# Performance work log

Measured on AMD Instinct MI355X. Metric: run time of the kernel, lower is better.

The kernel has to match this reference:

```python
import jax, jax.numpy as jnp
import numpy as np

B, NP, DIM = 32, 1369, 768
NCLS, K = 200, 5
C = NCLS + 1          # n_classes + background
H = W = 37            # sqrt(NP)
GAMMA = 0.99
SCALE = 4.0
SINKHORN_ITERS = 3
PCA_ITERS = 10
PCA_THRESH = 0.5
EPS = 1e-8


def _l2norm(x):
    return x / jnp.clip(jnp.linalg.norm(x, axis=-1, keepdims=True), EPS)


def setup_inputs() -> dict:
    key = jax.random.key(0)
    k1, k2, k3 = jax.random.split(key, 3)
    patch_tokens = jax.random.normal(k1, (B, NP, DIM), dtype=jnp.float32)
    labels = jax.random.randint(k2, (B,), 0, NCLS)
    prototypes = 0.02 * jax.random.normal(k3, (C, K, DIM), dtype=jnp.float32)  # trunc_normal std=0.02 approx
    sa = jnp.full((NCLS, K), 0.5, dtype=jnp.float32)
    scale = jnp.asarray(SCALE, dtype=jnp.float32)
    return {"patch_tokens": patch_tokens, "labels": labels,
            "prototypes": prototypes, "sa": sa, "scale": scale}


def reference(patch_tokens, labels, prototypes, sa, scale):
    # --- cosine patch-prototype similarity ---
    tok_n = _l2norm(patch_tokens)                 # [B, NP, D]
    pro_n = _l2norm(prototypes)                   # [C, K, D]
    logits = scale * jnp.einsum('bnd,ckd->bnck', tok_n, pro_n)  # [B, NP, C, K]

    # --- avg pooling + 'sa' classification head ---
    image_logits = logits.mean(axis=1)            # [B, C, K]
    sa_w = jax.nn.softmax(sa, axis=-1) * K        # [NCLS, K]
    class_logits = (image_logits[:, :NCLS, :] * sa_w).sum(axis=-1)  # [B, NCLS]

    # --- PCA pseudo patch labels (power iteration, q=1, centered) ---
    X = jax.lax.stop_gradient(patch_tokens).reshape(-1, DIM)  # [N, D]
    Xc = X - X.mean(axis=0, keepdims=True)
    v = jax.random.normal(jax.random.key(42), (DIM,), dtype=jnp.float32)
    for _ in range(PCA_ITERS):
        u = Xc @ v
        v = Xc.T @ u
        v = v / jnp.clip(jnp.linalg.norm(v), EPS)
    u = Xc @ v
    U = u / jnp.clip(jnp.linalg.norm(u), EPS)     # leading left singular vector
    U_scaled = (U - U.min()) / jnp.clip(U.max() - U.min(), EPS)
    U_img = U_scaled.reshape(B, H, W)
    pseudo = jnp.where(U_img <= PCA_THRESH,
                       labels[:, None, None],
                       C - 1).astype(jnp.int32)   # [B, H, W]

    # --- online clustering: masked sinkhorn vectorized over classes ---
    flat_lab = pseudo.reshape(-1)                 # [N]
    cls_ids = jnp.arange(C)
    mask = (flat_lab[:, None] == cls_ids[None, :]).astype(jnp.float32)  # [N, C]
    Nc = mask.sum(axis=0)                         # [C] fg patch count per class
    Lf = jax.lax.stop_gradient(logits).reshape(-1, C, K)
    Q = jnp.exp(Lf) * mask[:, :, None]            # [N, C, K], zero outside class mask
    Q = Q / jnp.clip(Q.sum(axis=(0, 2)), EPS)[None, :, None]
    Ncc = jnp.clip(Nc, 1.0)
    for _ in range(SINKHORN_ITERS):
        Q = Q / jnp.clip(Q.sum(axis=0), EPS)[None] / K           # col normalize
        Q = Q / jnp.clip(Q.sum(axis=2, keepdims=True), EPS) / Ncc[None, :, None]  # row normalize
    Q = Q * Nc[None, :, None]
    tok_flat = jax.lax.stop_gradient(tok_n).reshape(-1, DIM)
    P_new = jnp.einsum('nck,nd->ckd', Q, tok_flat)               # [C, K, D]
    updated = GAMMA * prototypes + (1.0 - GAMMA) * P_new          # momentum update
    present = jnp.isin(cls_ids, labels)                           # classes in this batch
    new_prototypes = jnp.where(present[:, None, None], updated, prototypes)

    return (logits, image_logits, class_logits, pseudo, new_prototypes)
```

## Files before the change

### kernel.cpp

```cpp
#include <hip/hip_runtime.h>

constexpr int   BB    = 32;
constexpr int   NPP   = 1369;
constexpr int   DIMC  = 768;
constexpr int   NCLSC = 200;
constexpr int   KP    = 5;
constexpr int   CC    = 201;
constexpr int   CKC   = 1005;
constexpr int   NPAD  = 1024;
constexpr int   NTOK  = BB * NPP;
constexpr float EPSF  = 1e-8f;
constexpr int   PWIN  = 128;
constexpr int   MTILES = 343;
constexpr int   NSLAB = 4;

typedef __attribute__((ext_vector_type(8))) short bf16x8;
typedef __attribute__((ext_vector_type(4))) float f32x4;

constexpr size_t O_LOG = 0;
constexpr size_t O_IMG = (size_t)NTOK * CKC;
constexpr size_t O_CLS = O_IMG + (size_t)BB * CKC;
constexpr size_t O_PSE = O_CLS + (size_t)BB * NCLSC;
constexpr size_t O_PRO = O_PSE + (size_t)NTOK;

constexpr size_t W_PRONBF = 0;
constexpr size_t W_INVN   = W_PRONBF + (size_t)NPAD*DIMC/2;
constexpr size_t W_MU     = W_INVN + NTOK;
constexpr size_t W_COLS   = W_MU + 2*DIMC;
constexpr size_t W_VBUF   = W_COLS + 2*NSLAB*DIMC;
constexpr size_t W_SSUM   = W_VBUF + 2*11*NSLAB*DIMC;
constexpr size_t W_TSUM   = W_SSUM + 128;
constexpr size_t W_NC     = W_TSUM + CC;
constexpr size_t W_FILL   = W_NC + CC;
constexpr size_t W_PRES   = W_FILL + CC;
constexpr size_t ZG_LEN   = (W_PRES + CC) - W_COLS;
constexpr size_t W_CSQ    = W_PRES + CC;
constexpr size_t W_U      = ((W_CSQ + CKC) + 1) & ~(size_t)1;
constexpr size_t W_PART   = W_U + 2*NTOK;
constexpr size_t W_SCAL   = W_PART + 2*1536;
constexpr size_t W_Q      = W_SCAL + 16;
constexpr size_t W_PNEW   = W_Q + (size_t)NTOK*KP;
constexpr size_t W_PLAB   = W_PNEW + (size_t)CC*KP*DIMC;
constexpr size_t W_OFFS   = W_PLAB + NTOK;
constexpr size_t W_RLST   = W_OFFS + 256;
constexpr size_t W_XBF    = ((W_RLST + NTOK) + 3) & ~(size_t)3;
constexpr size_t W_END_BIG  = W_XBF + (size_t)(NTOK + 128)*DIMC/2;
constexpr size_t W_PRON32   = W_XBF;
constexpr size_t W_END_FALL = W_PRON32 + (size_t)CKC*DIMC;

__device__ __forceinline__ unsigned short f2bf(float x) {
    unsigned u = __float_as_uint(x);
    unsigned r = (u + 0x7fffu + ((u >> 16) & 1u)) >> 16;
    return (unsigned short)r;
}

typedef __attribute__((address_space(3))) unsigned int as3_u32;
typedef __attribute__((address_space(1))) unsigned int as1_u32;
__device__ __forceinline__ void gload16(const unsigned short* g, unsigned short* l) {
    __builtin_amdgcn_global_load_lds((as1_u32*)g, (as3_u32*)l, 16, 0, 0);
}

__global__ void fill_zero(float* p, int n) {
    int i = blockIdx.x * 256 + threadIdx.x;
    if (i < n) p[i] = 0.0f;
}

__global__ __launch_bounds__(256) void tok_stats(const float* __restrict__ X,
                                                 float* __restrict__ invn,
                                                 double* __restrict__ colsD,
                                                 unsigned short* __restrict__ xbf) {
    __shared__ double csh[4][768];
    const int tid  = threadIdx.x;
    const int lane = tid & 63;
    const int wid  = tid >> 6;
    const int gw   = blockIdx.x * 4 + wid;
    double cacc[3][4];
    #pragma unroll
    for (int j = 0; j < 3; j++)
        #pragma unroll
        for (int t = 0; t < 4; t++) cacc[j][t] = 0.0;
    for (int n = gw; n < NTOK; n += 4096) {
        const float4* row = (const float4*)(X + (size_t)n * DIMC);
        float s = 0.0f;
        float4 xv[3];
        #pragma unroll
        for (int j = 0; j < 3; j++) {
            xv[j] = row[lane + 64*j];
            s = fmaf(xv[j].x, xv[j].x, s); s = fmaf(xv[j].y, xv[j].y, s);
            s = fmaf(xv[j].z, xv[j].z, s); s = fmaf(xv[j].w, xv[j].w, s);
            cacc[j][0] += (double)xv[j].x; cacc[j][1] += (double)xv[j].y;
            cacc[j][2] += (double)xv[j].z; cacc[j][3] += (double)xv[j].w;
        }
        if (xbf) {
            unsigned short* orow = xbf + (size_t)n * DIMC;
            #pragma unroll
            for (int j = 0; j < 3; j++) {
                ushort4 pk;
                pk.x = f2bf(xv[j].x); pk.y = f2bf(xv[j].y);
                pk.z = f2bf(xv[j].z); pk.w = f2bf(xv[j].w);
                *(ushort4*)(orow + 4*(lane + 64*j)) = pk;
            }
        }
        #pragma unroll
        for (int o = 32; o >= 1; o >>= 1) s += __shfl_xor(s, o);
        if (lane == 0) invn[n] = 1.0f / fmaxf(sqrtf(s), EPSF);
    }
    #pragma unroll
    for (int j = 0; j < 3; j++)
        #pragma unroll
        for (int t = 0; t < 4; t++)
            csh[wid][4*lane + 256*j + t] = cacc[j][t];
    __syncthreads();
    const int slab = blockIdx.x & (NSLAB - 1);
    for (int c = tid; c < 768; c += 256)
        atomicAdd(&colsD[slab * 768 + c], csh[0][c] + csh[1][c] + csh[2][c] + csh[3][c]);
}

__global__ __launch_bounds__(256) void proto_norm(const float* __restrict__ P,
                                                  unsigned short* __restrict__ pbf,
                                                  float* __restrict__ p32) {
    const int lane = threadIdx.x & 63;
    const int gw   = blockIdx.x * 4 + (threadIdx.x >> 6);
    for (int j = gw; j < NPAD; j += 256) {
        unsigned short* obf = pbf + (size_t)j * DIMC;
        if (j >= CKC) {
            #pragma unroll
            for (int t = 0; t < 12; t++) obf[lane + 64*t] = 0;
            continue;
        }
        const float* row = P + (size_t)j * DIMC;
        float x[12]; float s = 0.0f;
        #pragma unroll
        for (int t = 0; t < 12; t++) { x[t] = row[lane + 64*t]; s = fmaf(x[t], x[t], s); }
        #pragma unroll
        for (int o = 32; o >= 1; o >>= 1) s += __shfl_xor(s, o);
        float nrm = fmaxf(sqrtf(s), EPSF);
        #pragma unroll
        for (int t = 0; t < 12; t++) {
            float nv = x[t] / nrm;
            obf[lane + 64*t] = f2bf(nv);
            if (p32) p32[(size_t)j * DIMC + lane + 64*t] = nv;
        }
    }
}

__global__ __launch_bounds__(256) void logits_gemm(
        const unsigned short* __restrict__ Xbf,
        const unsigned short* __restrict__ Pbf,
        const float* __restrict__ invn,
        const float* __restrict__ scale_p,
        float* __restrict__ out,
        float* __restrict__ img) {
    __shared__ unsigned short As[128 * 32];
    __shared__ unsigned short Bs[128 * 32];
    const int b   = blockIdx.x;
    const int swz = (b & 7) * MTILES + (b >> 3);
    const int row_t = swz >> 3, col_t = swz & 7;
    const int row0 = row_t * 128, col0 = col_t * 128;
    const int tid = threadIdx.x, lane = tid & 63, wid = tid >> 6;
    const int wm = (wid >> 1) * 64, wn = (wid & 1) * 64;
    const int fr = lane & 15, fq = lane >> 4;

    f32x4 acc[4][4] = {};

    const int w32 = wid * 32;
    const int lrow = lane >> 2;
    const int gch = ((lane & 3) ^ ((lrow ^ (lrow >> 2)) & 3)) * 8;
    const unsigned short* aS0 = Xbf + (size_t)(row0 + w32 + lrow) * DIMC + gch;
    const unsigned short* aS1 = aS0 + (size_t)16 * DIMC;
    const unsigned short* bS0 = Pbf + (size_t)(col0 + w32 + lrow) * DIMC + gch;
    const unsigned short* bS1 = bS0 + (size_t)16 * DIMC;
    unsigned short* aD0 = &As[(w32)      * 32];
    unsigned short* aD1 = &As[(w32 + 16) * 32];
    unsigned short* bD0 = &Bs[(w32)      * 32];
    unsigned short* bD1 = &Bs[(w32 + 16) * 32];

    const int rc = (fq ^ ((fr ^ (fr >> 2)) & 3)) * 8;

    for (int ks = 0; ks < DIMC / 32; ks++) {
        __syncthreads();
        gload16(aS0 + ks * 32, aD0);
        gload16(aS1 + ks * 32, aD1);
        gload16(bS0 + ks * 32, bD0);
        gload16(bS1 + ks * 32, bD1);
        __syncthreads();
        bf16x8 af[4], bfr[4];
        #pragma unroll
        for (int m = 0; m < 4; m++)
            af[m] = *(const bf16x8*)(As + (wm + m * 16 + fr) * 32 + rc);
        #pragma unroll
        for (int n = 0; n < 4; n++)
            bfr[n] = *(const bf16x8*)(Bs + (wn + n * 16 + fr) * 32 + rc);
        #pragma unroll
        for (int m = 0; m < 4; m++)
            #pragma unroll
            for (int n = 0; n < 4; n++)
                acc[m][n] = __builtin_amdgcn_mfma_f32_16x16x32_bf16(af[m], bfr[n], acc[m][n], 0, 0, 0);
    }

    const float sc = *scale_p;
    #pragma unroll
    for (int m = 0; m < 4; m++) {
        const int rbase = row0 + wm + m * 16 + fq * 4;
        float fin[4];
        #pragma unroll
        for (int rr = 0; rr < 4; rr++) {
            int rrow = rbase + rr;
            fin[rr] = (rrow < NTOK) ? sc * invn[rrow] : 0.0f;
        }
        const int strip0 = row0 + wm + m * 16;
        const bool sameImg = ((strip0 / NPP) == ((strip0 + 15) / NPP)) && (strip0 + 15) < NTOK;
        const int bimg = strip0 / NPP;
        #pragma unroll
        for (int n = 0; n < 4; n++) {
            const int col = col0 + wn + n * 16 + fr;
            const bool cok = col < CKC;
            float csum = 0.0f;
            #pragma unroll
            for (int rr = 0; rr < 4; rr++) {
                int rrow = rbase + rr;
                float v = fin[rr] * acc[m][n][rr];
                if (cok && rrow < NTOK) out[(size_t)rrow * CKC + col] = v;
                csum += v;
            }
            if (sameImg) {
                csum += __shfl_xor(csum, 16);
                csum += __shfl_xor(csum, 32);
                if (lane < 16 && cok) atomicAdd(&img[bimg * CKC + col], csum);
            } else if (cok) {
                #pragma unroll
                for (int rr = 0; rr < 4; rr++) {
                    int rrow = rbase + rr;
                    if (rrow < NTOK)
                        atomicAdd(&img[(rrow / NPP) * CKC + col], fin[rr] * acc[m][n][rr]);
                }
            }
        }
    }
}

__global__ __launch_bounds__(256) void gemm_logits(const float* __restrict__ X,
                                                   const float* __restrict__ Bn,
                                                   const float* __restrict__ invn,
                                                   const float* __restrict__ scale_p,
                                                   float* __restrict__ out) {
    __shared__ float As[32][68];
    __shared__ float Bs[32][68];
    const int tid = threadIdx.x;
    const int tx = tid & 15, ty = tid >> 4;
    const int row0 = blockIdx.x * 64;
    const int col0 = blockIdx.y * 64;
    const int lm = tid >> 2;
    const int kb = (tid & 3) * 8;
    float acc[4][4] = {};
    for (int k0 = 0; k0 < DIMC; k0 += 32) {
        float a[8], b[8];
        int ar = row0 + lm;
        if (ar < NTOK) {
            const float* ap = X + (size_t)ar * DIMC + k0 + kb;
            #pragma unroll
            for (int j = 0; j < 8; j++) a[j] = ap[j];
        } else {
            #pragma unroll
            for (int j = 0; j < 8; j++) a[j] = 0.0f;
        }
        int bc = col0 + lm;
        if (bc < CKC) {
            const float* bp = Bn + (size_t)bc * DIMC + k0 + kb;
            #pragma unroll
            for (int j = 0; j < 8; j++) b[j] = bp[j];
        } else {
            #pragma unroll
            for (int j = 0; j < 8; j++) b[j] = 0.0f;
        }
        __syncthreads();
        #pragma unroll
        for (int j = 0; j < 8; j++) As[kb + j][lm] = a[j];
        #pragma unroll
        for (int j = 0; j < 8; j++) Bs[kb + j][lm] = b[j];
        __syncthreads();
        #pragma unroll
        for (int kk = 0; kk < 32; kk++) {
            float av[4], bv[4];
            #pragma unroll
            for (int i = 0; i < 4; i++) av[i] = As[kk][ty*4 + i];
            #pragma unroll
            for (int j = 0; j < 4; j++) bv[j] = Bs[kk][tx*4 + j];
            #pragma unroll
            for (int i = 0; i < 4; i++)
                #pragma unroll
                for (int j = 0; j < 4; j++)
                    acc[i][j] = fmaf(av[i], bv[j], acc[i][j]);
        }
    }
    const float sc = *scale_p;
    #pragma unroll
    for (int i = 0; i < 4; i++) {
        int r = row0 + ty*4 + i;
        if (r >= NTOK) continue;
        float f = sc * invn[r];
        float* orow = out + (size_t)r * CKC;
        #pragma unroll
        for (int j = 0; j < 4; j++) {
            int c = col0 + tx*4 + j;
            if (c < CKC) orow[c] = f * acc[i][j];
        }
    }
}

__global__ void img_reduce(const float* __restrict__ logits, float* __restrict__ img) {
    int b = blockIdx.x, jc = blockIdx.y, nc = blockIdx.z;
    int j = jc * 256 + threadIdx.x;
    if (j >= CKC) return;
    int p0 = nc * 172, p1 = min(NPP, p0 + 172);
    const float* base = logits + (size_t)b * NPP * CKC + j;
    float s = 0.0f;
    for (int p = p0; p < p1; p++) s += base[(size_t)p * CKC];
    atomicAdd(&img[b * CKC + j], s);
}

__global__ __launch_bounds__(256) void img_final(float* __restrict__ img,
                                                 const float* __restrict__ sa,
                                                 float* __restrict__ cls) {
    int b = blockIdx.x;
    for (int i = threadIdx.x; i < CKC; i += 256)
        img[b * CKC + i] = img[b * CKC + i] / 1369.0f;
    __syncthreads();
    for (int c = threadIdx.x; c < NCLSC; c += 256) {
        float vv[KP]; float mx = -3.4e38f;
        #pragma unroll
        for (int k = 0; k < KP; k++) { vv[k] = sa[c * KP + k]; mx = fmaxf(mx, vv[k]); }
        float e[KP]; float s = 0.0f;
        #pragma unroll
        for (int k = 0; k < KP; k++) { e[k] = expf(vv[k] - mx); s += e[k]; }
        float cl = 0.0f;
        #pragma unroll
        for (int k = 0; k < KP; k++) {
            float sw = e[k] / s * 5.0f;
            cl += img[b * CKC + c * KP + k] * sw;
        }
        cls[b * NCLSC + c] = cl;
    }
}

__global__ void mu_final(const double* __restrict__ colsD, double* __restrict__ mu) {
    int d = threadIdx.x;
    mu[d] = (colsD[d] + colsD[768 + d] + colsD[1536 + d] + colsD[2304 + d]) / (double)NTOK;
}

__device__ __forceinline__ float bits_to_normal(unsigned bits) {
    float f = __uint_as_float((bits >> 9) | 0x3f800000u) - 1.0f;
    const float lo = -0.99999994f;
    float u = f * 2.0f + lo;
    u = fmaxf(lo, u);
    float w = -log1pf(-u * u);
    float p;
    if (w < 5.0f) {
        w -= 2.5f;
        p = 2.81022636e-08f;
        p = fmaf(p, w, 3.43273939e-07f);
        p = fmaf(p, w, -3.5233877e-06f);
        p = fmaf(p, w, -4.39150654e-06f);
        p = fmaf(p, w, 0.00021858087f);
        p = fmaf(p, w, -0.00125372503f);
        p = fmaf(p, w, -0.00417768164f);
        p = fmaf(p, w, 0.246640727f);
        p = fmaf(p, w, 1.50140941f);
    } else {
        w = sqrtf(w) - 3.0f;
        p = -0.000200214257f;
        p = fmaf(p, w, 0.000100950558f);
        p = fmaf(p, w, 0.00134934322f);
        p = fmaf(p, w, -0.00367342844f);
        p = fmaf(p, w, 0.00573950773f);
        p = fmaf(p, w, -0.0076224613f);
        p = fmaf(p, w, 0.00943887047f);
        p = fmaf(p, w, 1.00167406f);
        p = fmaf(p, w, 2.83297682f);
    }
    return 1.41421356237f * (p * u);
}

#define TF_ROUND(r) { x0 += x1; x1 = (x1 << r) | (x1 >> (32 - r)); x1 ^= x0; }
__global__ void v0_gen(double* __restrict__ v) {
    int i = blockIdx.x * 256 + threadIdx.x;
    if (i >= DIMC) return;
    unsigned x0 = 0u, x1 = (unsigned)i;
    const unsigned k0 = 0u, k1 = 42u, k2 = k0 ^ k1 ^ 0x1BD11BDAu;
    x0 += k0; x1 += k1;
    TF_ROUND(13) TF_ROUND(15) TF_ROUND(26) TF_ROUND(6)
    x0 += k1; x1 += k2 + 1u;
    TF_ROUND(17) TF_ROUND(29) TF_ROUND(16) TF_ROUND(24)
    x0 += k2; x1 += k0 + 2u;
    TF_ROUND(13) TF_ROUND(15) TF_ROUND(26) TF_ROUND(6)
    x0 += k0; x1 += k1 + 3u;
    TF_ROUND(17) TF_ROUND(29) TF_ROUND(16) TF_ROUND(24)
    x0 += k1; x1 += k2 + 4u;
    TF_ROUND(13) TF_ROUND(15) TF_ROUND(26) TF_ROUND(6)
    x0 += k2; x1 += k0 + 5u;
    v[i] = (double)bits_to_normal(x0 ^ x1);
}

__global__ __launch_bounds__(256) void pca_pass(const float* __restrict__ X,
                                                const double* __restrict__ mu,
                                                const double* __restrict__ vraw,
                                                const double* __restrict__ Sin,
                                                double* __restrict__ vnext,
                                                double* __restrict__ Snext) {
    __shared__ double wacc[4][768];
    __shared__ double redw[4];
    const int tid = threadIdx.x, lane = tid & 63, wid = tid >> 6;
    const double S = Sin[0] + Sin[1] + Sin[2] + Sin[3];
    double ver[3][4];
    double mv = 0.0;
    #pragma unroll
    for (int j = 0; j < 3; j++)
        #pragma unroll
        for (int t = 0; t < 4; t++) {
            int c = 4*lane + 256*j + t;
            double x = (vraw[c] + vraw[768 + c] + vraw[1536 + c] + vraw[2304 + c]) - S * mu[c];
            ver[j][t] = x;
            mv += mu[c] * x;
        }
    #pragma unroll
    for (int o = 32; o >= 1; o >>= 1) mv += __shfl_xor(mv, o);
    const double muv = mv;

    double acc[3][4] = {};
    double usum = 0.0;
    const int gw = blockIdx.x * 4 + wid;
    for (int n0 = gw; n0 < NTOK; n0 += 4096) {
        const int n1 = n0 + 2048;
        const bool h1 = (n1 < NTOK);
        const float4* r0 = (const float4*)(X + (size_t)n0 * DIMC);
        const float4* r1 = (const float4*)(X + (size_t)(h1 ? n1 : n0) * DIMC);
        float4 xa[3], xb[3];
        #pragma unroll
        for (int j = 0; j < 3; j++) xa[j] = r0[lane + 64*j];
        #pragma unroll
        for (int j = 0; j < 3; j++) xb[j] = r1[lane + 64*j];
        double s0 = 0.0, s1 = 0.0;
        #pragma unroll
        for (int j = 0; j < 3; j++) {
            s0 = fma((double)xa[j].x, ver[j][0], s0);
            s0 = fma((double)xa[j].y, ver[j][1], s0);
            s0 = fma((double)xa[j].z, ver[j][2], s0);
            s0 = fma((double)xa[j].w, ver[j][3], s0);
            s1 = fma((double)xb[j].x, ver[j][0], s1);
            s1 = fma((double)xb[j].y, ver[j][1], s1);
            s1 = fma((double)xb[j].z, ver[j][2], s1);
            s1 = fma((double)xb[j].w, ver[j][3], s1);
        }
        #pragma unroll
        for (int o = 32; o >= 1; o >>= 1) { s0 += __shfl_xor(s0, o); s1 += __shfl_xor(s1, o); }
        double uu0 = s0 - muv;
        usum += uu0;
        #pragma unroll
        for (int j = 0; j < 3; j++) {
            acc[j][0] = fma((double)xa[j].x, uu0, acc[j][0]);
            acc[j][1] = fma((double)xa[j].y, uu0, acc[j][1]);
            acc[j][2] = fma((double)xa[j].z, uu0, acc[j][2]);
            acc[j][3] = fma((double)xa[j].w, uu0, acc[j][3]);
        }
        if (h1) {
            double uu1 = s1 - muv;
            usum += uu1;
            #pragma unroll
            for (int j = 0; j < 3; j++) {
                acc[j][0] = fma((double)xb[j].x, uu1, acc[j][0]);
                acc[j][1] = fma((double)xb[j].y, uu1, acc[j][1]);
                acc[j][2] = fma((double)xb[j].z, uu1, acc[j][2]);
                acc[j][3] = fma((double)xb[j].w, uu1, acc[j][3]);
            }
        }
    }
    #pragma unroll
    for (int j = 0; j < 3; j++)
        #pragma unroll
        for (int t = 0; t < 4; t++)
            wacc[wid][4*lane + 256*j + t] = acc[j][t];
    if (lane == 0) redw[wid] = usum;
    __syncthreads();
    const int slab = blockIdx.x & (NSLAB - 1);
    for (int c = tid; c < 768; c += 256)
        atomicAdd(&vnext[slab * 768 + c], wacc[0][c] + wacc[1][c] + wacc[2][c] + wacc[3][c]);
    if (tid == 0) atomicAdd(&Snext[slab], redw[0] + redw[1] + redw[2] + redw[3]);
}

__global__ __launch_bounds__(256) void u_final(const float* __restrict__ X,
                                               const double* __restrict__ mu,
                                               const double* __restrict__ vraw,
                                               const double* __restrict__ Sin,
                                               double* __restrict__ u,
                                               double* __restrict__ part) {
    __shared__ double wmin[4], wmax[4], wss[4];
    const int tid = threadIdx.x, lane = tid & 63, wid = tid >> 6;
    const double S = Sin[0] + Sin[1] + Sin[2] + Sin[3];
    double ver[3][4];
    double mv = 0.0;
    #pragma unroll
    for (int j = 0; j < 3; j++)
        #pragma unroll
        for (int t = 0; t < 4; t++) {
            int c = 4*lane + 256*j + t;
            double x = (vraw[c] + vraw[768 + c] + vraw[1536 + c] + vraw[2304 + c]) - S * mu[c];
            ver[j][t] = x;
            mv += mu[c] * x;
        }
    #pragma unroll
    for (int o = 32; o >= 1; o >>= 1) mv += __shfl_xor(mv, o);
    const double muv = mv;
    double lmin = 1e300, lmax = -1e300, lss = 0.0;
    for (int n = blockIdx.x * 4 + wid; n < NTOK; n += 2048) {
        const float4* row = (const float4*)(X + (size_t)n * DIMC);
        double s = 0.0;
        #pragma unroll
        for (int j = 0; j < 3; j++) {
            float4 xv = row[lane + 64*j];
            s = fma((double)xv.x, ver[j][0], s);
            s = fma((double)xv.y, ver[j][1], s);
            s = fma((double)xv.z, ver[j][2], s);
            s = fma((double)xv.w, ver[j][3], s);
        }
        #pragma unroll
        for (int o = 32; o >= 1; o >>= 1) s += __shfl_xor(s, o);
        double uu = s - muv;
        if (lane == 0) {
            u[n] = uu;
            lmin = fmin(lmin, uu); lmax = fmax(lmax, uu); lss = fma(uu, uu, lss);
        }
    }
    if (lane == 0) { wmin[wid] = lmin; wmax[wid] = lmax; wss[wid] = lss; }
    __syncthreads();
    if (tid == 0) {
        part[blockIdx.x]        = fmin(fmin(wmin[0], wmin[1]), fmin(wmin[2], wmin[3]));
        part[512 + blockIdx.x]  = fmax(fmax(wmax[0], wmax[1]), fmax(wmax[2], wmax[3]));
        part[1024 + blockIdx.x] = wss[0] + wss[1] + wss[2] + wss[3];
    }
}

__global__ __launch_bounds__(512) void final_scalars(const double* __restrict__ part,
                                                     double* __restrict__ scal,
                                                     const int* __restrict__ labels,
                                                     int* __restrict__ pres) {
    __shared__ double rmin[512], rmax[512], rss[512];
    int t = threadIdx.x;
    rmin[t] = part[t]; rmax[t] = part[512 + t]; rss[t] = part[1024 + t];
    __syncthreads();
    for (int s = 256; s > 0; s >>= 1) {
        if (t < s) {
            rmin[t] = fmin(rmin[t], rmin[t + s]);
            rmax[t] = fmax(rmax[t], rmax[t + s]);
            rss[t] += rss[t + s];
        }
        __syncthreads();
    }
    if (t == 0) {
        double nrm = fmax(sqrt(rss[0]), 1e-8);
        double Umin = rmin[0] / nrm;
        double Umax = rmax[0] / nrm;
        scal[1] = nrm;
        scal[2] = Umin;
        scal[3] = fmax(Umax - Umin, 1e-8);
    }
    if (t < BB) pres[labels[t]] = 1;
}

__global__ __launch_bounds__(256) void pseudo_kernel(
        const double* __restrict__ u, const double* __restrict__ scal,
        const int* __restrict__ labels, float* __restrict__ pse,
        int* __restrict__ plab, int* __restrict__ Nc) {
    __shared__ int hist[CC];
    const int tid = threadIdx.x;
    for (int c = tid; c < CC; c += 256) hist[c] = 0;
    __syncthreads();
    int n = blockIdx.x * 256 + tid;
    if (n < NTOK) {
        double U  = u[n] / scal[1];
        double Us = (U - scal[2]) / scal[3];
        int lab = (Us <= 0.5) ? labels[n / NPP] : (CC - 1);
        pse[n] = (float)lab;
        plab[n] = lab;
        atomicAdd(&hist[lab], 1);
    }
    __syncthreads();
    for (int c = tid; c < CC; c += 256)
        if (hist[c] > 0) atomicAdd(&Nc[c], hist[c]);
}

__global__ void offs_scan(const int* __restrict__ Nc, int* __restrict__ offs) {
    if (threadIdx.x == 0) {
        int s = 0;
        for (int c = 0; c < CC; c++) { offs[c] = s; s += Nc[c]; }
        offs[CC] = s;
    }
}

__global__ __launch_bounds__(256) void scatter_rows(
        const int* __restrict__ plab, const int* __restrict__ offs,
        int* __restrict__ fill, int* __restrict__ rlist) {
    __shared__ int hist[CC];
    __shared__ int base[CC];
    const int tid = threadIdx.x;
    for (int c = tid; c < CC; c += 256) hist[c] = 0;
    __syncthreads();
    int n = blockIdx.x * 256 + tid;
    int lab = -1, posl = 0;
    if (n < NTOK) {
        lab = plab[n];
        posl = atomicAdd(&hist[lab], 1);
    }
    __syncthreads();
    for (int c = tid; c < CC; c += 256) {
        int h = hist[c];
        if (h > 0) base[c] = atomicAdd(&fill[c], h);
    }
    __syncthreads();
    if (n < NTOK) rlist[offs[lab] + base[lab] + posl] = n;
}

__global__ __launch_bounds__(256) void sinkhorn_fused(
        const float* __restrict__ logits,
        const int* __restrict__ offs,
        const int* __restrict__ rlist,
        float* __restrict__ qseg) {
    const int c  = blockIdx.x;
    const int i0 = offs[c], i1 = offs[c + 1];
    const int cnt = i1 - i0;
    if (cnt <= 0) return;
    const int tid = threadIdx.x;
    __shared__ float cs[KP];
    __shared__ float redk[KP][4];

    for (int i = i0 + tid; i < i1; i += 256) {
        int n = rlist[i];
        const float* lp = logits + (size_t)n * CKC + c * KP;
        #pragma unroll
        for (int k = 0; k < KP; k++) qseg[(size_t)i * KP + k] = expf(lp[k]);
    }
    const float Ncc = fmaxf((float)cnt, 1.0f);
    for (int it = 0; it < 3; it++) {
        __syncthreads();
        float lc[KP] = {};
        for (int i = i0 + tid; i < i1; i += 256) {
            #pragma unroll
            for (int k = 0; k < KP; k++) lc[k] += qseg[(size_t)i * KP + k];
        }
        #pragma unroll
        for (int k = 0; k < KP; k++) {
            float v = lc[k];
            #pragma unroll
            for (int o = 32; o >= 1; o >>= 1) v += __shfl_xor(v, o);
            if ((tid & 63) == 0) redk[k][tid >> 6] = v;
        }
        __syncthreads();
        if (tid == 0) {
            #pragma unroll
            for (int k = 0; k < KP; k++)
                cs[k] = fmaxf(redk[k][0] + redk[k][1] + redk[k][2] + redk[k][3], EPSF) * 5.0f;
        }
        __syncthreads();
        float inv_cs[KP];
        #pragma unroll
        for (int k = 0; k < KP; k++) inv_cs[k] = 1.0f / cs[k];
        const float outsc = (it == 2) ? ((float)cnt / Ncc) : (1.0f / Ncc);
        for (int i = i0 + tid; i < i1; i += 256) {
            float v[KP]; float rs = 0.0f;
            #pragma unroll
            for (int k = 0; k < KP; k++) { v[k] = qseg[(size_t)i*KP + k] * inv_cs[k]; rs += v[k]; }
            float f = outsc / fmaxf(rs, EPSF);
            #pragma unroll
            for (int k = 0; k < KP; k++) qseg[(size_t)i*KP + k] = v[k] * f;
        }
    }
}

__global__ __launch_bounds__(256) void pnew_partial(
        const float* __restrict__ X,
        const float* __restrict__ invn,
        const float* __restrict__ qseg,
        const int* __restrict__ offs,
        const int* __restrict__ rlist,
        const int* __restrict__ plab,
        float* __restrict__ Pnew) {
    const int d = blockIdx.y * 256 + threadIdx.x;
    const int fgEnd = offs[CC - 1];
    int i0 = blockIdx.x * PWIN;
    if (i0 >= fgEnd) return;
    int i1 = min(i0 + PWIN, fgEnd);
    int curlab = -1;
    float acc[KP] = {};
    for (int i = i0; i < i1; i++) {
        int n = rlist[i];
        int lab = plab[n];
        if (lab != curlab) {
            if (curlab >= 0) {
                #pragma unroll
                for (int k = 0; k < KP; k++)
                    atomicAdd(&Pnew[((size_t)curlab * KP + k) * DIMC + d], acc[k]);
            }
            curlab = lab;
            #pragma unroll
            for (int k = 0; k < KP; k++) acc[k] = 0.0f;
        }
        float x = X[(size_t)n * DIMC + d] * invn[n];
        #pragma unroll
        for (int k = 0; k < KP; k++) acc[k] = fmaf(qseg[(size_t)i * KP + k], x, acc[k]);
    }
    if (curlab >= 0) {
        #pragma unroll
        for (int k = 0; k < KP; k++)
            atomicAdd(&Pnew[((size_t)curlab * KP + k) * DIMC + d], acc[k]);
    }
}

__global__ void proto_out(const float* __restrict__ proto, const float* __restrict__ Pnew,
                          const int* __restrict__ pres, float* __restrict__ outp) {
    int idx = blockIdx.x * 256 + threadIdx.x;
    if (idx >= CC * KP * DIMC) return;
    int c = idx / (KP * DIMC);
    float p = proto[idx];
    float r = p;
    if (pres[c]) {
        const float g = 0.99f;
        r = g * p + (1.0f - g) * Pnew[idx];
    }
    outp[idx] = r;
}

extern "C" void kernel_launch(void* const* d_in, const int* in_sizes, int n_in,
                              void* d_out, int out_size, void* d_ws, size_t ws_size,
                              hipStream_t stream) {
    const float* X      = (const float*)d_in[0];
    const int*   labels = (const int*)  d_in[1];
    const float* proto  = (const float*)d_in[2];
    const float* sa     = (const float*)d_in[3];
    const float* scale  = (const float*)d_in[4];
    float* out = (float*)d_out;
    float* ws  = (float*)d_ws;
    const bool big = ws_size >= W_END_BIG * sizeof(float);
    if (!big && ws_size < W_END_FALL * sizeof(float)) return;

    unsigned short* pronbf = (unsigned short*)(ws + W_PRONBF);
    float*  invn  = ws + W_INVN;
    double* mu    = (double*)(ws + W_MU);
    double* colsD = (double*)(ws + W_COLS);
    double* vbuf  = (double*)(ws + W_VBUF);
    double* Ssum  = (double*)(ws + W_SSUM);
    int*    Nc    = (int*)(ws + W_NC);
    int*    fill  = (int*)(ws + W_FILL);
    int*    pres  = (int*)(ws + W_PRES);
    double* u     = (double*)(ws + W_U);
    double* part  = (double*)(ws + W_PART);
    double* scal  = (double*)(ws + W_SCAL);
    float*  qseg  = ws + W_Q;
    float*  Pnew  = ws + W_PNEW;
    int*    plab  = (int*)(ws + W_PLAB);
    int*    offs  = (int*)(ws + W_OFFS);
    int*    rlist = (int*)(ws + W_RLST);
    unsigned short* xbf = big ? (unsigned short*)(ws + W_XBF) : nullptr;
    float*  pron32 = big ? nullptr : (ws + W_PRON32);

    fill_zero<<<((int)ZG_LEN + 255) / 256, 256, 0, stream>>>(ws + W_COLS, (int)ZG_LEN);
    fill_zero<<<(CC * KP * DIMC + 255) / 256, 256, 0, stream>>>(Pnew, CC * KP * DIMC);
    fill_zero<<<(BB * CKC + 255) / 256, 256, 0, stream>>>(out + O_IMG, BB * CKC);

    tok_stats<<<1024, 256, 0, stream>>>(X, invn, colsD, xbf);
    proto_norm<<<64, 256, 0, stream>>>(proto, pronbf, pron32);
    if (big) {
        logits_gemm<<<MTILES * 8, 256, 0, stream>>>(xbf, pronbf, invn, scale,
                                                    out + O_LOG, out + O_IMG);
    } else {
        gemm_logits<<<dim3(685, 16), 256, 0, stream>>>(X, pron32, invn, scale, out + O_LOG);
        img_reduce<<<dim3(32, 4, 8), 256, 0, stream>>>(out + O_LOG, out + O_IMG);
    }
    img_final<<<32, 256, 0, stream>>>(out + O_IMG, sa, out + O_CLS);

    mu_final<<<1, 768, 0, stream>>>(colsD, mu);
    v0_gen<<<3, 256, 0, stream>>>(vbuf);
    for (int t = 0; t < 10; t++) {
        pca_pass<<<512, 256, 0, stream>>>(X, mu,
            vbuf + (size_t)t * NSLAB * DIMC, Ssum + t * NSLAB,
            vbuf + (size_t)(t + 1) * NSLAB * DIMC, Ssum + (t + 1) * NSLAB);
    }
    u_final<<<512, 256, 0, stream>>>(X, mu,
        vbuf + (size_t)10 * NSLAB * DIMC, Ssum + 10 * NSLAB, u, part);
    final_scalars<<<1, 512, 0, stream>>>(part, scal, labels, pres);
    pseudo_kernel<<<172, 256, 0, stream>>>(u, scal, labels, out + O_PSE, plab, Nc);

    offs_scan<<<1, 64, 0, stream>>>(Nc, offs);
    scatter_rows<<<172, 256, 0, stream>>>(plab, offs, fill, rlist);
    sinkhorn_fused<<<NCLSC, 256, 0, stream>>>(out + O_LOG, offs, rlist, qseg);
    pnew_partial<<<dim3((NTOK + PWIN - 1) / PWIN, 3), 256, 0, stream>>>(
        X, invn, qseg, offs, rlist, plab, Pnew);
    proto_out<<<(CC * KP * DIMC + 255) / 256, 256, 0, stream>>>(proto, Pnew, pres, out + O_PRO);
}
```

Measured before the change: 599.0 us.

## Double GEMM K-tile to 64 and widen PCA passes to 8 slabs

The logits GEMM now stages 64-wide K slices in LDS with an XOR swizzle over 8 chunks. Each tile feeds two MFMA sub-steps, which halves the number of barrier pairs per K loop. The PCA power-iteration passes launch twice as many blocks and spread their atomics over 8 partial slabs instead of 4, to raise occupancy and cut atomic contention. LDS use per GEMM block doubles, and the reductions now sum 8 partials. One risk is that tok_stats' column partials may still be written for 4 slabs while mu_final now reads 8.

```diff
diff --git a/kernel.cpp b/kernel.cpp
--- a/kernel.cpp
+++ b/kernel.cpp
@@ -12,7 +12,7 @@
 constexpr float EPSF  = 1e-8f;
 constexpr int   PWIN  = 128;
 constexpr int   MTILES = 343;
-constexpr int   NSLAB = 4;
+constexpr int   NSLAB = 8;
 
 typedef __attribute__((ext_vector_type(8))) short bf16x8;
 typedef __attribute__((ext_vector_type(4))) float f32x4;
@@ -29,7 +29,7 @@
 constexpr size_t W_COLS   = W_MU + 2*DIMC;
 constexpr size_t W_VBUF   = W_COLS + 2*NSLAB*DIMC;
 constexpr size_t W_SSUM   = W_VBUF + 2*11*NSLAB*DIMC;
-constexpr size_t W_TSUM   = W_SSUM + 128;
+constexpr size_t W_TSUM   = W_SSUM + 256;
 constexpr size_t W_NC     = W_TSUM + CC;
 constexpr size_t W_FILL   = W_NC + CC;
 constexpr size_t W_PRES   = W_FILL + CC;
@@ -151,8 +151,8 @@
         const float* __restrict__ scale_p,
         float* __restrict__ out,
         float* __restrict__ img) {
-    __shared__ unsigned short As[128 * 32];
-    __shared__ unsigned short Bs[128 * 32];
+    __shared__ unsigned short As[128 * 64];
+    __shared__ unsigned short Bs[128 * 64];
     const int b   = blockIdx.x;
     const int swz = (b & 7) * MTILES + (b >> 3);
     const int row_t = swz >> 3, col_t = swz & 7;
@@ -164,38 +164,36 @@
     f32x4 acc[4][4] = {};
 
     const int w32 = wid * 32;
-    const int lrow = lane >> 2;
-    const int gch = ((lane & 3) ^ ((lrow ^ (lrow >> 2)) & 3)) * 8;
-    const unsigned short* aS0 = Xbf + (size_t)(row0 + w32 + lrow) * DIMC + gch;
-    const unsigned short* aS1 = aS0 + (size_t)16 * DIMC;
-    const unsigned short* bS0 = Pbf + (size_t)(col0 + w32 + lrow) * DIMC + gch;
-    const unsigned short* bS1 = bS0 + (size_t)16 * DIMC;
-    unsigned short* aD0 = &As[(w32)      * 32];
-    unsigned short* aD1 = &As[(w32 + 16) * 32];
-    unsigned short* bD0 = &Bs[(w32)      * 32];
-    unsigned short* bD1 = &Bs[(w32 + 16) * 32];
-
-    const int rc = (fq ^ ((fr ^ (fr >> 2)) & 3)) * 8;
-
-    for (int ks = 0; ks < DIMC / 32; ks++) {
+    const int lr8 = lane >> 3;
+    const int lch = (lane & 7) ^ lr8;
+    const unsigned short* aBase = Xbf + (size_t)(row0 + w32 + lr8) * DIMC + lch * 8;
+    const unsigned short* bBase = Pbf + (size_t)(col0 + w32 + lr8) * DIMC + lch * 8;
+
+    for (int ks = 0; ks < DIMC / 64; ks++) {
         __syncthreads();
-        gload16(aS0 + ks * 32, aD0);
-        gload16(aS1 + ks * 32, aD1);
-        gload16(bS0 + ks * 32, bD0);
-        gload16(bS1 + ks * 32, bD1);
+        #pragma unroll
+        for (int i = 0; i < 4; i++) {
+            gload16(aBase + (size_t)(8 * i) * DIMC + ks * 64, &As[(w32 + 8 * i) * 64]);
+            gload16(bBase + (size_t)(8 * i) * DIMC + ks * 64, &Bs[(w32 + 8 * i) * 64]);
+        }
         __syncthreads();
-        bf16x8 af[4], bfr[4];
-        #pragma unroll
-        for (int m = 0; m < 4; m++)
-            af[m] = *(const bf16x8*)(As + (wm + m * 16 + fr) * 32 + rc);
-        #pragma unroll
-        for (int n = 0; n < 4; n++)
-            bfr[n] = *(const bf16x8*)(Bs + (wn + n * 16 + fr) * 32 + rc);
-        #pragma unroll
-        for (int m = 0; m < 4; m++)
+        #pragma unroll
+        for (int kk = 0; kk < 2; kk++) {
+            bf16x8 af[4], bfr[4];
+            #pragma unroll
+            for (int m = 0; m < 4; m++)
+                af[m] = *(const bf16x8*)(As + (wm + m * 16 + fr) * 64 +
+                                         (((kk << 2) | fq) ^ (fr & 7)) * 8);
             #pragma unroll
             for (int n = 0; n < 4; n++)
-                acc[m][n] = __builtin_amdgcn_mfma_f32_16x16x32_bf16(af[m], bfr[n], acc[m][n], 0, 0, 0);
+                bfr[n] = *(const bf16x8*)(Bs + (wn + n * 16 + fr) * 64 +
+                                          (((kk << 2) | fq) ^ (fr & 7)) * 8);
+            #pragma unroll
+            for (int m = 0; m < 4; m++)
+                #pragma unroll
+                for (int n = 0; n < 4; n++)
+                    acc[m][n] = __builtin_amdgcn_mfma_f32_16x16x32_bf16(af[m], bfr[n], acc[m][n], 0, 0, 0);
+        }
     }
 
     const float sc = *scale_p;
@@ -345,7 +343,10 @@
 
 __global__ void mu_final(const double* __restrict__ colsD, double* __restrict__ mu) {
     int d = threadIdx.x;
-    mu[d] = (colsD[d] + colsD[768 + d] + colsD[1536 + d] + colsD[2304 + d]) / (double)NTOK;
+    double s = 0.0;
+    #pragma unroll
+    for (int k = 0; k < NSLAB; k++) s += colsD[k * 768 + d];
+    mu[d] = s / (double)NTOK;
 }
 
 __device__ __forceinline__ float bits_to_normal(unsigned bits) {
@@ -410,7 +411,9 @@
     __shared__ double wacc[4][768];
     __shared__ double redw[4];
     const int tid = threadIdx.x, lane = tid & 63, wid = tid >> 6;
-    const double S = Sin[0] + Sin[1] + Sin[2] + Sin[3];
+    double S = 0.0;
+    #pragma unroll
+    for (int k = 0; k < NSLAB; k++) S += Sin[k];
     double ver[3][4];
     double mv = 0.0;
     #pragma unroll
@@ -418,7 +421,10 @@
         #pragma unroll
         for (int t = 0; t < 4; t++) {
             int c = 4*lane + 256*j + t;
-            double x = (vraw[c] + vraw[768 + c] + vraw[1536 + c] + vraw[2304 + c]) - S * mu[c];
+            double vr = 0.0;
+            #pragma unroll
+            for (int k = 0; k < NSLAB; k++) vr += vraw[k * 768 + c];
+            double x = vr - S * mu[c];
             ver[j][t] = x;
             mv += mu[c] * x;
         }
@@ -429,8 +435,8 @@
     double acc[3][4] = {};
     double usum = 0.0;
     const int gw = blockIdx.x * 4 + wid;
-    for (int n0 = gw; n0 < NTOK; n0 += 4096) {
-        const int n1 = n0 + 2048;
+    for (int n0 = gw; n0 < NTOK; n0 += 8192) {
+        const int n1 = n0 + 4096;
         const bool h1 = (n1 < NTOK);
         const float4* r0 = (const float4*)(X + (size_t)n0 * DIMC);
         const float4* r1 = (const float4*)(X + (size_t)(h1 ? n1 : n0) * DIMC);
@@ -495,7 +501,9 @@
                                                double* __restrict__ part) {
     __shared__ double wmin[4], wmax[4], wss[4];
     const int tid = threadIdx.x, lane = tid & 63, wid = tid >> 6;
-    const double S = Sin[0] + Sin[1] + Sin[2] + Sin[3];
+    double S = 0.0;
+    #pragma unroll
+    for (int k = 0; k < NSLAB; k++) S += Sin[k];
     double ver[3][4];
     double mv = 0.0;
     #pragma unroll
@@ -503,7 +511,10 @@
         #pragma unroll
         for (int t = 0; t < 4; t++) {
             int c = 4*lane + 256*j + t;
-            double x = (vraw[c] + vraw[768 + c] + vraw[1536 + c] + vraw[2304 + c]) - S * mu[c];
+            double vr = 0.0;
+            #pragma unroll
+            for (int k = 0; k < NSLAB; k++) vr += vraw[k * 768 + c];
+            double x = vr - S * mu[c];
             ver[j][t] = x;
             mv += mu[c] * x;
         }
@@ -779,7 +790,7 @@
     mu_final<<<1, 768, 0, stream>>>(colsD, mu);
     v0_gen<<<3, 256, 0, stream>>>(vbuf);
     for (int t = 0; t < 10; t++) {
-        pca_pass<<<512, 256, 0, stream>>>(X, mu,
+        pca_pass<<<1024, 256, 0, stream>>>(X, mu,
             vbuf + (size_t)t * NSLAB * DIMC, Ssum + t * NSLAB,
             vbuf + (size_t)(t + 1) * NSLAB * DIMC, Ssum + (t + 1) * NSLAB);
     }
```

Result: slower. 628.5 us (+4.9%).
